# Kernel tuning notes

Measured on AMD Instinct MI355X. Metric: run time of the kernel, lower is better.

Reference implementation:

```python
import jax, jax.numpy as jnp
import numpy as np

N = 50000
E = 800000
IN_CH = 64
OUT_CH = 64
K = 2  # kernel_size (dim=1, degree=1 B-spline -> linear interpolation)


def setup_inputs() -> dict:
    key = jax.random.key(0)
    k1, k2, k3, k4, k5, k6 = jax.random.split(key, 6)
    x = jax.random.normal(k1, (N, IN_CH), dtype=jnp.float32)
    edge_index = jax.random.randint(k2, (2, E), 0, N, dtype=jnp.int64)
    edge_attr = jax.random.uniform(k3, (E, 1), dtype=jnp.float32)  # pseudo coords in [0,1]
    scale = 1.0 / np.sqrt(IN_CH)
    weight = jax.random.normal(k4, (K, IN_CH, OUT_CH), dtype=jnp.float32) * scale
    root = jax.random.normal(k5, (IN_CH, OUT_CH), dtype=jnp.float32) * scale
    bias = jax.random.normal(k6, (OUT_CH,), dtype=jnp.float32) * 0.01
    return {"x": x, "edge_index": edge_index, "edge_attr": edge_attr,
            "weight": weight, "root": root, "bias": bias}


def reference(x, edge_index, edge_attr, weight, root, bias):
    # SplineConv, dim=1, kernel_size=2, degree=1, open spline, aggr='mean',
    # root_weight=True, bias=True. Followed by ReLU; dropout is identity (eval mode).
    src, dst = edge_index[0], edge_index[1]
    u = edge_attr[:, 0]                      # [E], pseudo in [0,1]
    v = u * (K - 1)
    i0 = jnp.clip(jnp.floor(v).astype(jnp.int32), 0, K - 1)
    i1 = jnp.clip(i0 + 1, 0, K - 1)
    f = v - jnp.floor(v)                     # fractional part -> linear basis (1-f, f)
    # Precompute x @ W_k for each kernel index: [K, N, OUT]
    xw = jnp.einsum('ni,kio->kno', x, weight)
    # Per-edge weighted message: [E, OUT]
    m = (1.0 - f)[:, None] * xw[i0, src] + f[:, None] * xw[i1, src]
    # Mean aggregation at target nodes
    agg = jax.ops.segment_sum(m, dst, num_segments=N)
    cnt = jax.ops.segment_sum(jnp.ones((E,), dtype=x.dtype), dst, num_segments=N)
    out = agg / jnp.maximum(cnt, 1.0)[:, None]
    out = out + x @ root + bias
    return jax.nn.relu(out)
```

## Files before the change

kernel.cpp:

```cpp
#include <hip/hip_runtime.h>
#include <hip/hip_bf16.h>
#include <hip/hip_fp16.h>

#define CH 64
#define BSHIFT 7
#define BINSZ 128
#define BCAP 3072
#define EPB 4096
#define MAXBINS 400

typedef _Float16 f16x8 __attribute__((ext_vector_type(8)));
typedef float f32x4 __attribute__((ext_vector_type(4)));
typedef float f32x2 __attribute__((ext_vector_type(2)));

__global__ __launch_bounds__(256) void prepw_kernel(
        const float* __restrict__ w,
        const float* __restrict__ root,
        _Float16* __restrict__ WT,
        int* __restrict__ bin_cursor, int n_bins) {
    const int t = threadIdx.x;
    for (int i = t; i < n_bins; i += 256) bin_cursor[i] = 0;
    for (int id = t; id < 192 * 8; id += 256) {
        int n = id >> 3, c = id & 7;
        const float* src = (n < 128) ? (w + (n >> 6) * 4096 + (n & 63))
                                     : (root + (n - 128));
        f16x8 v;
#pragma unroll
        for (int j = 0; j < 8; ++j) v[j] = (_Float16)src[(c * 8 + j) * 64];
        *(f16x8*)(WT + n * 64 + c * 8) = v;
    }
}

__device__ __forceinline__ void mfma_body(
        int bb, const float* __restrict__ x, const _Float16* __restrict__ WT,
        const float* __restrict__ bias, unsigned short* __restrict__ xwp,
        __half* __restrict__ base, int n_nodes) {
    const int wave = threadIdx.x >> 6, lane = threadIdx.x & 63;
    const int m0 = bb * 64 + wave * 16;
    const int c = lane & 15, g = lane >> 4;
    int arow = m0 + c; if (arow > n_nodes - 1) arow = n_nodes - 1;
    const float* xr = x + (size_t)arow * CH + g * 8;
    f32x4 v0 = *(const f32x4*)(xr);
    f32x4 v1 = *(const f32x4*)(xr + 4);
    f32x4 v2 = *(const f32x4*)(xr + 32);
    f32x4 v3 = *(const f32x4*)(xr + 36);
    f16x8 a0, a1;
#pragma unroll
    for (int j = 0; j < 4; ++j) {
        a0[j] = (_Float16)v0[j]; a0[4 + j] = (_Float16)v1[j];
        a1[j] = (_Float16)v2[j]; a1[4 + j] = (_Float16)v3[j];
    }
    f32x4 acc[12];
#pragma unroll
    for (int nt = 0; nt < 12; ++nt) acc[nt] = (f32x4){0.f, 0.f, 0.f, 0.f};
#pragma unroll
    for (int nt = 0; nt < 12; ++nt) {
        int n = nt * 16 + c;
        f16x8 b0 = *(const f16x8*)(WT + n * 64 + g * 8);
        f16x8 b1 = *(const f16x8*)(WT + n * 64 + 32 + g * 8);
        acc[nt] = __builtin_amdgcn_mfma_f32_16x16x32_f16(a0, b0, acc[nt], 0, 0, 0);
        acc[nt] = __builtin_amdgcn_mfma_f32_16x16x32_f16(a1, b1, acc[nt], 0, 0, 0);
    }
    float bv[4];
#pragma unroll
    for (int gr = 0; gr < 4; ++gr) bv[gr] = bias[gr * 16 + c];
#pragma unroll
    for (int reg = 0; reg < 4; ++reg) {
        int node = m0 + g * 4 + reg;
        if (node < n_nodes) {
#pragma unroll
            for (int gr = 0; gr < 4; ++gr) {
                int ch = gr * 16 + c;
                int pk = __builtin_amdgcn_cvt_pk_fp8_f32(
                    acc[gr][reg], acc[gr + 4][reg], 0, false);
                xwp[(size_t)node * CH + ch] = (unsigned short)(pk & 0xFFFF);
                base[(size_t)node * CH + ch] = __float2half(acc[gr + 8][reg] + bv[gr]);
            }
        }
    }
}

__global__ __launch_bounds__(256) void fused_kernel(
        const float* __restrict__ x, const _Float16* __restrict__ WT,
        const float* __restrict__ bias,
        const int* __restrict__ ei, const float* __restrict__ ea,
        int* __restrict__ bin_cursor, unsigned int* __restrict__ binned,
        unsigned short* __restrict__ xwp, __half* __restrict__ base,
        int n_nodes, int n_edges, int n_bins, int part_blocks) {
    __shared__ uint2 sh[EPB];
    __shared__ int hist[MAXBINS], bstart[MAXBINS + 1];
    __shared__ int gbase[MAXBINS], lcur[MAXBINS];
    if (blockIdx.x >= part_blocks) {
        mfma_body(blockIdx.x - part_blocks, x, WT, bias, xwp, base, n_nodes);
        return;
    }
    const int t = threadIdx.x;
    for (int i = t; i < n_bins; i += 256) hist[i] = 0;
    __syncthreads();
    const int e0 = blockIdx.x * EPB;
    uint2 rec[EPB / 256];
#pragma unroll
    for (int k = 0; k < EPB / 256; ++k) {
        int e = e0 + k * 256 + t;
        if (e < n_edges) {
            int s = ei[e];
            int d = ei[n_edges + e];
            float u = ea[e];
            float fl = floorf(u);
            int i0 = max(0, min((int)fl, 1));
            int i1 = min(i0 + 1, 1);
            float f = u - fl;
            float a1 = ((i0 == 1) ? (1.f - f) : 0.f) + ((i1 == 1) ? f : 0.f);
            unsigned q = __float2uint_rn(a1 * 255.f);
            unsigned dloc = (unsigned)(d & (BINSZ - 1));
            rec[k] = make_uint2((unsigned)s | (q << 16) | (dloc << 24), (unsigned)d);
            atomicAdd(&hist[d >> BSHIFT], 1);
        } else {
            rec[k] = make_uint2(0u, 0xFFFFFFFFu);
        }
    }
    __syncthreads();
    if (t < 64) {
        int carry = 0;
        for (int b = 0; b < n_bins; b += 64) {
            int i = b + t;
            int v = (i < n_bins) ? hist[i] : 0;
            int incl = v;
#pragma unroll
            for (int off = 1; off < 64; off <<= 1) {
                int nv = __shfl_up(incl, off);
                if (t >= off) incl += nv;
            }
            if (i < n_bins) bstart[i] = incl - v + carry;
            carry += __shfl(incl, 63);
        }
        if (t == 0) bstart[n_bins] = carry;
    }
    __syncthreads();
    for (int i = t; i < n_bins; i += 256) {
        int cnt = hist[i];
        gbase[i] = cnt ? atomicAdd(&bin_cursor[i], cnt) : 0;
        lcur[i] = bstart[i];
    }
    __syncthreads();
#pragma unroll
    for (int k = 0; k < EPB / 256; ++k) {
        if (rec[k].y != 0xFFFFFFFFu) {
            int b = (int)(rec[k].y >> BSHIFT);
            int p = atomicAdd(&lcur[b], 1);
            sh[p] = rec[k];
        }
    }
    __syncthreads();
    int total = bstart[n_bins];
    for (int idx = t; idx < total; idx += 256) {
        uint2 r = sh[idx];
        int b = (int)(r.y >> BSHIFT);
        int loc = gbase[b] + (idx - bstart[b]);
        if (loc < BCAP) binned[(size_t)b * BCAP + loc] = r.x;
    }
}

__global__ __launch_bounds__(256) void place2_kernel(
        const unsigned int* __restrict__ binned,
        const int* __restrict__ bin_count,
        unsigned int* __restrict__ csr,
        int* __restrict__ offs,
        int n_nodes, int n_bins, int n_edges) {
    __shared__ int dcnt[BINSZ];
    __shared__ int dbase[BINSZ];
    __shared__ int dcur[BINSZ];
    __shared__ int base_sh;
    const int bin = blockIdx.x;
    const int t = threadIdx.x;
    if (t < 64) {
        int s = 0;
        for (int i = t; i < bin; i += 64) s += bin_count[i];
#pragma unroll
        for (int off = 32; off > 0; off >>= 1) s += __shfl_down(s, off);
        if (t == 0) base_sh = s;
    }
    if (bin == 0 && t == 0) offs[n_nodes] = n_edges;
    if (t < BINSZ) dcnt[t] = 0;
    __syncthreads();
    const int base = base_sh;
    int cnt = bin_count[bin]; if (cnt > BCAP) cnt = BCAP;
    unsigned int rec[BCAP / 256];
#pragma unroll
    for (int k = 0; k < BCAP / 256; ++k) {
        int i = k * 256 + t;
        if (i < cnt) {
            rec[k] = binned[(size_t)bin * BCAP + i];
            atomicAdd(&dcnt[rec[k] >> 24], 1);
        }
    }
    __syncthreads();
    if (t < 64) {
        int carry = 0;
        for (int b = 0; b < BINSZ; b += 64) {
            int i = b + t;
            int v = dcnt[i];
            int incl = v;
#pragma unroll
            for (int off = 1; off < 64; off <<= 1) {
                int nv = __shfl_up(incl, off);
                if (t >= off) incl += nv;
            }
            dbase[i] = incl - v + carry;
            carry += __shfl(incl, 63);
        }
    }
    __syncthreads();
    if (t < BINSZ) {
        dcur[t] = dbase[t];
        int node = (bin << BSHIFT) + t;
        if (node < n_nodes) offs[node] = base + dbase[t];
    }
    __syncthreads();
#pragma unroll
    for (int k = 0; k < BCAP / 256; ++k) {
        int i = k * 256 + t;
        if (i < cnt) {
            int d = rec[k] >> 24;
            int p = atomicAdd(&dcur[d], 1);
            csr[base + p] = rec[k] & 0x00FFFFFFu;
        }
    }
}

__global__ void gather_kernel(const int* __restrict__ offs,
                              const unsigned int* __restrict__ recs,
                              const unsigned short* __restrict__ xwp,
                              const __half* __restrict__ base,
                              float* __restrict__ out,
                              int n_nodes) {
    int wid = (blockIdx.x * blockDim.x + threadIdx.x) >> 6;
    int lane = threadIdx.x & 63;
    if (wid >= n_nodes) return;
    int beg = offs[wid], end = offs[wid + 1];
    float acc = 0.f;
    const float qs = 1.f / 255.f;
    for (int tb = beg; tb < end; tb += 64) {
        int n = end - tb; if (n > 64) n = 64;
        int r = 0;
        if (lane < n) r = (int)recs[tb + lane];
        int j = 0;
        for (; j + 4 <= n; j += 4) {
            int p0 = __shfl(r, j),     p1 = __shfl(r, j + 1);
            int p2 = __shfl(r, j + 2), p3 = __shfl(r, j + 3);
            float u0 = (float)(((unsigned)p0 >> 16) & 255u) * qs;
            float u1 = (float)(((unsigned)p1 >> 16) & 255u) * qs;
            float u2 = (float)(((unsigned)p2 >> 16) & 255u) * qs;
            float u3 = (float)(((unsigned)p3 >> 16) & 255u) * qs;
            f32x2 a = __builtin_amdgcn_cvt_pk_f32_fp8(
                (int)xwp[(size_t)(p0 & 0xFFFF) * CH + lane], false);
            f32x2 b = __builtin_amdgcn_cvt_pk_f32_fp8(
                (int)xwp[(size_t)(p1 & 0xFFFF) * CH + lane], false);
            f32x2 c = __builtin_amdgcn_cvt_pk_f32_fp8(
                (int)xwp[(size_t)(p2 & 0xFFFF) * CH + lane], false);
            f32x2 d = __builtin_amdgcn_cvt_pk_f32_fp8(
                (int)xwp[(size_t)(p3 & 0xFFFF) * CH + lane], false);
            acc += fmaf(u0, a[1] - a[0], a[0]);
            acc += fmaf(u1, b[1] - b[0], b[0]);
            acc += fmaf(u2, c[1] - c[0], c[0]);
            acc += fmaf(u3, d[1] - d[0], d[0]);
        }
        for (; j < n; ++j) {
            int p0 = __shfl(r, j);
            float u0 = (float)(((unsigned)p0 >> 16) & 255u) * qs;
            f32x2 a = __builtin_amdgcn_cvt_pk_f32_fp8(
                (int)xwp[(size_t)(p0 & 0xFFFF) * CH + lane], false);
            acc += fmaf(u0, a[1] - a[0], a[0]);
        }
    }
    int deg = end - beg;
    float c = (float)(deg > 0 ? deg : 1);
    size_t o = (size_t)wid * CH + lane;
    float val = acc / c + __half2float(base[o]);
    out[o] = fmaxf(val, 0.f);
}

extern "C" void kernel_launch(void* const* d_in, const int* in_sizes, int n_in,
                              void* d_out, int out_size, void* d_ws, size_t ws_size,
                              hipStream_t stream) {
    const float* x    = (const float*)d_in[0];
    const int*   ei   = (const int*)d_in[1];
    const float* ea   = (const float*)d_in[2];
    const float* w    = (const float*)d_in[3];
    const float* root = (const float*)d_in[4];
    const float* bias = (const float*)d_in[5];
    float* out = (float*)d_out;

    const int n_nodes = in_sizes[0] / CH;
    const int n_edges = in_sizes[2];
    const int n_bins  = (n_nodes + BINSZ - 1) >> BSHIFT;
    const int part_blocks = (n_edges + EPB - 1) / EPB;
    const int mfma_blocks = (n_nodes + 63) / 64;

    unsigned short* xwp  = (unsigned short*)d_ws;
    __half*       base   = (__half*)(xwp + (size_t)n_nodes * CH);
    unsigned int* binned = (unsigned int*)(base + (size_t)n_nodes * CH);
    unsigned int* csr    = binned + (size_t)n_bins * BCAP;
    _Float16*     WT     = (_Float16*)(csr + n_edges);
    int*          offs   = (int*)(WT + 192 * 64);
    int*          bin_cursor = offs + n_nodes + 1;

    prepw_kernel<<<1, 256, 0, stream>>>(w, root, WT, bin_cursor, n_bins);
    fused_kernel<<<part_blocks + mfma_blocks, 256, 0, stream>>>(
        x, WT, bias, ei, ea, bin_cursor, binned, xwp, base,
        n_nodes, n_edges, n_bins, part_blocks);
    place2_kernel<<<n_bins, 256, 0, stream>>>(binned, bin_cursor, csr, offs,
                                              n_nodes, n_bins, n_edges);
    gather_kernel<<<(n_nodes * CH + 255) / 256, 256, 0, stream>>>(
        offs, csr, xwp, base, out, n_nodes);
}
```

Baseline: 72.18 us.

## Fuse per-bin CSR placement with gather into one shared-memory kernel

Replaces the place2 and gather kernels with one kernel per destination bin of 1024 threads. It counting-sorts the bin's edge records in shared memory and has 16 waves aggregate the bin's nodes directly from that local CSR. This removes the global CSR and offsets writes and reads, the prefix sum over bin counts, and one kernel launch. The weight-prep kernel is also spread over 8 blocks. The trade-off is only 391 large blocks with about 25KB of LDS each, which may lower occupancy and load balance in the gather phase.

```diff
diff --git a/kernel.cpp b/kernel.cpp
--- a/kernel.cpp
+++ b/kernel.cpp
@@ -19,8 +19,10 @@
         _Float16* __restrict__ WT,
         int* __restrict__ bin_cursor, int n_bins) {
     const int t = threadIdx.x;
-    for (int i = t; i < n_bins; i += 256) bin_cursor[i] = 0;
-    for (int id = t; id < 192 * 8; id += 256) {
+    if (blockIdx.x == 0)
+        for (int i = t; i < n_bins; i += 256) bin_cursor[i] = 0;
+    const int gt = blockIdx.x * 256 + t;
+    for (int id = gt; id < 192 * 8; id += 2048) {
         int n = id >> 3, c = id & 7;
         const float* src = (n < 128) ? (w + (n >> 6) * 4096 + (n & 63))
                                      : (root + (n - 128));
@@ -161,38 +163,25 @@
     }
 }
 
-__global__ __launch_bounds__(256) void place2_kernel(
+__global__ __launch_bounds__(1024) void gatherbin_kernel(
         const unsigned int* __restrict__ binned,
         const int* __restrict__ bin_count,
-        unsigned int* __restrict__ csr,
-        int* __restrict__ offs,
-        int n_nodes, int n_bins, int n_edges) {
-    __shared__ int dcnt[BINSZ];
-    __shared__ int dbase[BINSZ];
-    __shared__ int dcur[BINSZ];
-    __shared__ int base_sh;
+        const unsigned short* __restrict__ xwp,
+        const __half* __restrict__ base,
+        float* __restrict__ out,
+        int n_nodes) {
+    __shared__ unsigned int raw[BCAP];
+    __shared__ unsigned int scsr[BCAP];
+    __shared__ int dcnt[BINSZ], dbase[BINSZ], dcur[BINSZ];
     const int bin = blockIdx.x;
     const int t = threadIdx.x;
-    if (t < 64) {
-        int s = 0;
-        for (int i = t; i < bin; i += 64) s += bin_count[i];
-#pragma unroll
-        for (int off = 32; off > 0; off >>= 1) s += __shfl_down(s, off);
-        if (t == 0) base_sh = s;
-    }
-    if (bin == 0 && t == 0) offs[n_nodes] = n_edges;
+    int cnt = bin_count[bin]; if (cnt > BCAP) cnt = BCAP;
     if (t < BINSZ) dcnt[t] = 0;
     __syncthreads();
-    const int base = base_sh;
-    int cnt = bin_count[bin]; if (cnt > BCAP) cnt = BCAP;
-    unsigned int rec[BCAP / 256];
-#pragma unroll
-    for (int k = 0; k < BCAP / 256; ++k) {
-        int i = k * 256 + t;
-        if (i < cnt) {
-            rec[k] = binned[(size_t)bin * BCAP + i];
-            atomicAdd(&dcnt[rec[k] >> 24], 1);
-        }
+    for (int i = t; i < cnt; i += 1024) {
+        unsigned r = binned[(size_t)bin * BCAP + i];
+        raw[i] = r;
+        atomicAdd(&dcnt[r >> 24], 1);
     }
     __syncthreads();
     if (t < 64) {
@@ -211,73 +200,59 @@
         }
     }
     __syncthreads();
-    if (t < BINSZ) {
-        dcur[t] = dbase[t];
-        int node = (bin << BSHIFT) + t;
-        if (node < n_nodes) offs[node] = base + dbase[t];
-    }
-    __syncthreads();
-#pragma unroll
-    for (int k = 0; k < BCAP / 256; ++k) {
-        int i = k * 256 + t;
-        if (i < cnt) {
-            int d = rec[k] >> 24;
-            int p = atomicAdd(&dcur[d], 1);
-            csr[base + p] = rec[k] & 0x00FFFFFFu;
-        }
-    }
-}
-
-__global__ void gather_kernel(const int* __restrict__ offs,
-                              const unsigned int* __restrict__ recs,
-                              const unsigned short* __restrict__ xwp,
-                              const __half* __restrict__ base,
-                              float* __restrict__ out,
-                              int n_nodes) {
-    int wid = (blockIdx.x * blockDim.x + threadIdx.x) >> 6;
-    int lane = threadIdx.x & 63;
-    if (wid >= n_nodes) return;
-    int beg = offs[wid], end = offs[wid + 1];
-    float acc = 0.f;
+    if (t < BINSZ) dcur[t] = dbase[t];
+    __syncthreads();
+    for (int i = t; i < cnt; i += 1024) {
+        unsigned r = raw[i];
+        int p = atomicAdd(&dcur[r >> 24], 1);
+        scsr[p] = r & 0x00FFFFFFu;
+    }
+    __syncthreads();
+    const int wave = t >> 6, lane = t & 63;
     const float qs = 1.f / 255.f;
-    for (int tb = beg; tb < end; tb += 64) {
-        int n = end - tb; if (n > 64) n = 64;
-        int r = 0;
-        if (lane < n) r = (int)recs[tb + lane];
-        int j = 0;
-        for (; j + 4 <= n; j += 4) {
-            int p0 = __shfl(r, j),     p1 = __shfl(r, j + 1);
-            int p2 = __shfl(r, j + 2), p3 = __shfl(r, j + 3);
-            float u0 = (float)(((unsigned)p0 >> 16) & 255u) * qs;
-            float u1 = (float)(((unsigned)p1 >> 16) & 255u) * qs;
-            float u2 = (float)(((unsigned)p2 >> 16) & 255u) * qs;
-            float u3 = (float)(((unsigned)p3 >> 16) & 255u) * qs;
-            f32x2 a = __builtin_amdgcn_cvt_pk_f32_fp8(
-                (int)xwp[(size_t)(p0 & 0xFFFF) * CH + lane], false);
-            f32x2 b = __builtin_amdgcn_cvt_pk_f32_fp8(
-                (int)xwp[(size_t)(p1 & 0xFFFF) * CH + lane], false);
-            f32x2 c = __builtin_amdgcn_cvt_pk_f32_fp8(
-                (int)xwp[(size_t)(p2 & 0xFFFF) * CH + lane], false);
-            f32x2 d = __builtin_amdgcn_cvt_pk_f32_fp8(
-                (int)xwp[(size_t)(p3 & 0xFFFF) * CH + lane], false);
-            acc += fmaf(u0, a[1] - a[0], a[0]);
-            acc += fmaf(u1, b[1] - b[0], b[0]);
-            acc += fmaf(u2, c[1] - c[0], c[0]);
-            acc += fmaf(u3, d[1] - d[0], d[0]);
-        }
-        for (; j < n; ++j) {
-            int p0 = __shfl(r, j);
-            float u0 = (float)(((unsigned)p0 >> 16) & 255u) * qs;
-            f32x2 a = __builtin_amdgcn_cvt_pk_f32_fp8(
-                (int)xwp[(size_t)(p0 & 0xFFFF) * CH + lane], false);
-            acc += fmaf(u0, a[1] - a[0], a[0]);
-        }
-    }
-    int deg = end - beg;
-    float c = (float)(deg > 0 ? deg : 1);
-    size_t o = (size_t)wid * CH + lane;
-    float val = acc / c + __half2float(base[o]);
-    out[o] = fmaxf(val, 0.f);
+    for (int dl = wave; dl < BINSZ; dl += 16) {
+        int node = (bin << BSHIFT) + dl;
+        if (node >= n_nodes) continue;
+        int deg = dcnt[dl];
+        int beg = dbase[dl], end = beg + deg;
+        float acc = 0.f;
+        for (int tb = beg; tb < end; tb += 64) {
+            int n = end - tb; if (n > 64) n = 64;
+            int r = 0;
+            if (lane < n) r = (int)scsr[tb + lane];
+            int j = 0;
+            for (; j + 4 <= n; j += 4) {
+                int p0 = __shfl(r, j),     p1 = __shfl(r, j + 1);
+                int p2 = __shfl(r, j + 2), p3 = __shfl(r, j + 3);
+                float u0 = (float)(((unsigned)p0 >> 16) & 255u) * qs;
+                float u1 = (float)(((unsigned)p1 >> 16) & 255u) * qs;
+                float u2 = (float)(((unsigned)p2 >> 16) & 255u) * qs;
+                float u3 = (float)(((unsigned)p3 >> 16) & 255u) * qs;
+                f32x2 a = __builtin_amdgcn_cvt_pk_f32_fp8(
+                    (int)xwp[(size_t)(p0 & 0xFFFF) * CH + lane], false);
+                f32x2 b = __builtin_amdgcn_cvt_pk_f32_fp8(
+                    (int)xwp[(size_t)(p1 & 0xFFFF) * CH + lane], false);
+                f32x2 c = __builtin_amdgcn_cvt_pk_f32_fp8(
+                    (int)xwp[(size_t)(p2 & 0xFFFF) * CH + lane], false);
+                f32x2 d = __builtin_amdgcn_cvt_pk_f32_fp8(
+                    (int)xwp[(size_t)(p3 & 0xFFFF) * CH + lane], false);
+                acc += fmaf(u0, a[1] - a[0], a[0]);
+                acc += fmaf(u1, b[1] - b[0], b[0]);
+                acc += fmaf(u2, c[1] - c[0], c[0]);
+                acc += fmaf(u3, d[1] - d[0], d[0]);
+            }
+            for (; j < n; ++j) {
+                int p0 = __shfl(r, j);
+                float u0 = (float)(((unsigned)p0 >> 16) & 255u) * qs;
+                f32x2 a = __builtin_amdgcn_cvt_pk_f32_fp8(
+                    (int)xwp[(size_t)(p0 & 0xFFFF) * CH + lane], false);
+                acc += fmaf(u0, a[1] - a[0], a[0]);
+            }
+        }
+        float c = (float)(deg > 0 ? deg : 1);
+        size_t o = (size_t)node * CH + lane;
+        out[o] = fmaxf(acc / c + __half2float(base[o]), 0.f);
+    }
 }
 
 extern "C" void kernel_launch(void* const* d_in, const int* in_sizes, int n_in,
@@ -300,17 +275,13 @@
     unsigned short* xwp  = (unsigned short*)d_ws;
     __half*       base   = (__half*)(xwp + (size_t)n_nodes * CH);
     unsigned int* binned = (unsigned int*)(base + (size_t)n_nodes * CH);
-    unsigned int* csr    = binned + (size_t)n_bins * BCAP;
-    _Float16*     WT     = (_Float16*)(csr + n_edges);
-    int*          offs   = (int*)(WT + 192 * 64);
-    int*          bin_cursor = offs + n_nodes + 1;
-
-    prepw_kernel<<<1, 256, 0, stream>>>(w, root, WT, bin_cursor, n_bins);
+    _Float16*     WT     = (_Float16*)(binned + (size_t)n_bins * BCAP);
+    int*          bin_cursor = (int*)(WT + 192 * 64);
+
+    prepw_kernel<<<8, 256, 0, stream>>>(w, root, WT, bin_cursor, n_bins);
     fused_kernel<<<part_blocks + mfma_blocks, 256, 0, stream>>>(
         x, WT, bias, ei, ea, bin_cursor, binned, xwp, base,
         n_nodes, n_edges, n_bins, part_blocks);
-    place2_kernel<<<n_bins, 256, 0, stream>>>(binned, bin_cursor, csr, offs,
-                                              n_nodes, n_bins, n_edges);
-    gather_kernel<<<(n_nodes * CH + 255) / 256, 256, 0, stream>>>(
-        offs, csr, xwp, base, out, n_nodes);
-}
+    gatherbin_kernel<<<n_bins, 1024, 0, stream>>>(binned, bin_cursor, xwp,
+                                                  base, out, n_nodes);
+}
```

Measured after the change: 64.77 us. 1.11x faster.
